# Kernel optimization log

Measured on AMD Instinct MI355X. Metric: run time of the kernel, lower is better.

The kernel has to match this reference:

```python
import jax, jax.numpy as jnp
import numpy as np

B, H, W, C, S, ITERS = 32, 80, 80, 32, 9, 3
HW = H * W
SCALE = C ** -0.5


def _grid(h, w):
    # matches SoftPositionEmbedding.build_grid: [1, h, w, 4] = [g, 1-g]
    r = jnp.stack(jnp.meshgrid(jnp.linspace(0., 1., h), jnp.linspace(0., 1., w), indexing='ij'), -1)
    return jnp.concatenate([r, 1. - r], -1)[None].astype(jnp.float32)


def _ln(x, g, b, ax):
    m = x.mean(ax, keepdims=True)
    v = x.var(ax, keepdims=True)
    return (x - m) / jnp.sqrt(v + 1e-5) * g + b


def _conv(x, w, b, p):
    y = jax.lax.conv_general_dilated(x, w, (1, 1), [(p, p), (p, p)],
                                     dimension_numbers=('NCHW', 'OIHW', 'NCHW'))
    return y + b[None, :, None, None]


def _convT(x, w, b, p):
    # stride-1 ConvTranspose2d == conv with spatially flipped kernel, pad k-1-p; w is [I,O,kh,kw]
    k = w.shape[-1]
    q = k - 1 - p
    y = jax.lax.conv_general_dilated(x, jnp.flip(w, (2, 3)), (1, 1), [(q, q), (q, q)],
                                     dimension_numbers=('NCHW', 'IOHW', 'NCHW'))
    return y + b[None, :, None, None]


def setup_inputs() -> dict:
    key = jax.random.key(0)
    ks = iter(jax.random.split(key, 64))

    def n(sh, s=0.05):
        return jax.random.normal(next(ks), sh, jnp.float32) * s

    return dict(
        x=jax.random.normal(next(ks), (B, 1, H, W), jnp.float32),
        slot_noise=jax.random.normal(next(ks), (B, S, C), jnp.float32),
        enc_w1=n((C, 1, 5, 5)), enc_b1=jnp.zeros((C,)),
        enc_w2=n((C, C, 5, 5)), enc_b2=jnp.zeros((C,)),
        enc_w3=n((C, C, 5, 5)), enc_b3=jnp.zeros((C,)),
        enc_w4=n((C, C, 5, 5)), enc_b4=jnp.zeros((C,)),
        pe_enc_w=n((C, 4)), pe_enc_b=jnp.zeros((C,)),
        ln_enc_g=jnp.ones((HW, C)), ln_enc_b=jnp.zeros((HW, C)),
        mlp_w1=n((C, C)), mlp_b1=jnp.zeros((C,)),
        mlp_w2=n((C, C)), mlp_b2=jnp.zeros((C,)),
        slots_mu=n((1, 1, C), 1.0), slots_sigma=jnp.abs(n((1, 1, C), 1.0)),
        ni_g=jnp.ones((C,)), ni_b=jnp.zeros((C,)),
        ns_g=jnp.ones((C,)), ns_b=jnp.zeros((C,)),
        q_w=n((C, C)), q_b=jnp.zeros((C,)),
        k_w=n((C, C)), k_b=jnp.zeros((C,)),
        v_w=n((C, C)), v_b=jnp.zeros((C,)),
        gru_wih=n((3 * C, C)), gru_whh=n((3 * C, C)),
        gru_bih=jnp.zeros((3 * C,)), gru_bhh=jnp.zeros((3 * C,)),
        res_ln_g=jnp.ones((C,)), res_ln_b=jnp.zeros((C,)),
        res_w1=n((C, C)), res_b1=jnp.zeros((C,)),
        res_w2=n((C, C)), res_b2=jnp.zeros((C,)),
        pe_dec_w=n((C, 4)), pe_dec_b=jnp.zeros((C,)),
        dec_w1=n((C, C, 5, 5)), dec_b1=jnp.zeros((C,)),
        dec_w2=n((C, C, 5, 5)), dec_b2=jnp.zeros((C,)),
        dec_w3=n((C, C, 5, 5)), dec_b3=jnp.zeros((C,)),
        dec_w4=n((C, 2, 3, 3)), dec_b4=jnp.zeros((2,)),
    )


def _forward(x, slot_noise, enc_w1, enc_b1, enc_w2, enc_b2, enc_w3, enc_b3, enc_w4, enc_b4,
             pe_enc_w, pe_enc_b, ln_enc_g, ln_enc_b, mlp_w1, mlp_b1, mlp_w2, mlp_b2,
             slots_mu, slots_sigma, ni_g, ni_b, ns_g, ns_b, q_w, q_b, k_w, k_b, v_w, v_b,
             gru_wih, gru_whh, gru_bih, gru_bhh, res_ln_g, res_ln_b, res_w1, res_b1,
             res_w2, res_b2, pe_dec_w, pe_dec_b, dec_w1, dec_b1, dec_w2, dec_b2,
             dec_w3, dec_b3, dec_w4, dec_b4):
    grid = _grid(H, W)  # [1,H,W,4]
    # --- conv encoder ---
    h = jax.nn.relu(_conv(x, enc_w1, enc_b1, 2))
    h = jax.nn.relu(_conv(h, enc_w2, enc_b2, 2))
    h = jax.nn.relu(_conv(h, enc_w3, enc_b3, 2))
    h = jax.nn.relu(_conv(h, enc_w4, enc_b4, 2))
    h = h.transpose(0, 2, 3, 1) + (grid @ pe_enc_w.T + pe_enc_b)  # soft pos emb
    h = h.reshape(B, HW, C)
    h = _ln(h, ln_enc_g, ln_enc_b, (-2, -1))  # LayerNorm([HW, C]): joint over last 2 dims
    h = jax.nn.relu(h @ mlp_w1.T + mlp_b1) @ mlp_w2.T + mlp_b2
    # --- slot attention ---
    slots = slots_mu + slots_sigma * slot_noise  # torch.normal(mu, sigma)
    xn = _ln(h, ni_g, ni_b, -1)
    keys = xn @ k_w.T + k_b
    values = xn @ v_w.T + v_b
    attn = None
    for _ in range(ITERS):
        prev = slots
        sn = _ln(slots, ns_g, ns_b, -1)
        q = sn @ q_w.T + q_b
        dots = jnp.einsum('bid,bjd->bij', q, keys) * SCALE  # [B,S,HW]
        attn = jax.nn.softmax(dots, axis=1) + 1e-8  # softmax over slots
        attn = attn / attn.sum(-1, keepdims=True)
        upd = jnp.einsum('bjd,bij->bid', values, attn)  # [B,S,C]
        # PyTorch GRUCell
        u2 = upd.reshape(-1, C)
        h2 = prev.reshape(-1, C)
        gx = u2 @ gru_wih.T + gru_bih
        gh = h2 @ gru_whh.T + gru_bhh
        xr, xz, xc = jnp.split(gx, 3, -1)
        hr, hz, hc = jnp.split(gh, 3, -1)
        r = jax.nn.sigmoid(xr + hr)
        z = jax.nn.sigmoid(xz + hz)
        cand = jnp.tanh(xc + r * hc)
        slots = ((1. - z) * cand + z * h2).reshape(B, S, C)
        res = _ln(slots, res_ln_g, res_ln_b, -1)
        res = jax.nn.relu(res @ res_w1.T + res_b1) @ res_w2.T + res_b2
        slots = slots + res
    # --- spatial-broadcast decoder ---
    d = jnp.broadcast_to(slots.reshape(B * S, 1, 1, C), (B * S, H, W, C))
    d = d + (grid @ pe_dec_w.T + pe_dec_b)
    d = d.transpose(0, 3, 1, 2)
    d = jax.nn.relu(_convT(d, dec_w1, dec_b1, 2))
    d = jax.nn.relu(_convT(d, dec_w2, dec_b2, 2))
    d = jax.nn.relu(_convT(d, dec_w3, dec_b3, 2))
    d = _convT(d, dec_w4, dec_b4, 1)
    d = d.transpose(0, 2, 3, 1).reshape(B, S, H, W, 2)
    recon, mlog = d[..., :1], d[..., 1:]
    mask = jax.nn.softmax(mlog, axis=1)  # over slots
    combined = (recon * mask).sum(1).transpose(0, 3, 1, 2)  # [B,1,H,W]
    return (combined, recon.transpose(0, 1, 4, 2, 3), mask.transpose(0, 1, 4, 2, 3),
            slots, attn.reshape(B, S, 1, H, W))


def reference(x, slot_noise, enc_w1, enc_b1, enc_w2, enc_b2, enc_w3, enc_b3, enc_w4, enc_b4,
              pe_enc_w, pe_enc_b, ln_enc_g, ln_enc_b, mlp_w1, mlp_b1, mlp_w2, mlp_b2,
              slots_mu, slots_sigma, ni_g, ni_b, ns_g, ns_b, q_w, q_b, k_w, k_b, v_w, v_b,
              gru_wih, gru_whh, gru_bih, gru_bhh, res_ln_g, res_ln_b, res_w1, res_b1,
              res_w2, res_b2, pe_dec_w, pe_dec_b, dec_w1, dec_b1, dec_w2, dec_b2,
              dec_w3, dec_b3, dec_w4, dec_b4):
    return _forward(x, slot_noise, enc_w1, enc_b1, enc_w2, enc_b2, enc_w3, enc_b3, enc_w4, enc_b4,
                    pe_enc_w, pe_enc_b, ln_enc_g, ln_enc_b, mlp_w1, mlp_b1, mlp_w2, mlp_b2,
                    slots_mu, slots_sigma, ni_g, ni_b, ns_g, ns_b, q_w, q_b, k_w, k_b, v_w, v_b,
                    gru_wih, gru_whh, gru_bih, gru_bhh, res_ln_g, res_ln_b, res_w1, res_b1,
                    res_w2, res_b2, pe_dec_w, pe_dec_b, dec_w1, dec_b1, dec_w2, dec_b2,
                    dec_w3, dec_b3, dec_w4, dec_b4)
```

## Files before the change

kernel.cpp:

```cpp
#include <hip/hip_runtime.h>
#include <cstddef>
#include <cstdint>


namespace {

constexpr int Bb  = 32;
constexpr int HWp = 6400;
constexpr float SCALEf = 0.17677669529663687f;

constexpr size_t O_COMB  = 0;
constexpr size_t O_RECON = 204800;
constexpr size_t O_MASK  = 2048000;
constexpr size_t O_SLOTS = 3891200;
constexpr size_t O_ATTN  = 3900416;

constexpr size_t W_PEENC = 0;
constexpr size_t W_PEDEC = 204800;
constexpr size_t W_BASE  = 409600;
constexpr size_t W_TC    = 512000;
constexpr size_t W_TS    = 537600;
constexpr size_t W_WP    = 768000;
constexpr size_t W_WPM   = 844800;
constexpr size_t W_LNPART= 846848;
constexpr size_t W_MEANR = 848448;
constexpr size_t W_Q     = 848512;
constexpr size_t W_SLOTS = 857728;
constexpr size_t W_APART = 866944;
constexpr size_t W_RSUM  = 874144;
constexpr size_t W_UP2   = 874432;
constexpr size_t W_KEYS  = 1104832;
constexpr size_t W_VALS  = 4381632;
constexpr size_t W_POOL  = 7658432;
constexpr size_t W_TOTAL = 29115328;

typedef __attribute__((ext_vector_type(8))) short short8;
typedef __attribute__((ext_vector_type(4))) float f32x4;

__device__ __forceinline__ ushort f2bf(float f) {
  uint u = __builtin_bit_cast(uint, f);
  uint r = (u + 0x7fffu + ((u >> 16) & 1u)) >> 16;
  return (ushort)r;
}
__device__ __forceinline__ float bf2f(ushort b) {
  uint u = ((uint)b) << 16;
  return __builtin_bit_cast(float, u);
}
__device__ __forceinline__ void unpk2(uint w, float& a, float& b) {
  a = __builtin_bit_cast(float, w << 16);
  b = __builtin_bit_cast(float, w & 0xffff0000u);
}

__device__ __forceinline__ void matvec32(const float* __restrict__ W,
                                         const float* __restrict__ bias,
                                         const float* x, float* y, bool relu) {
#pragma unroll
  for (int o = 0; o < 32; ++o) {
    float a = bias[o];
#pragma unroll
    for (int c = 0; c < 32; ++c) a = fmaf(x[c], W[o * 32 + c], a);
    y[o] = relu ? fmaxf(a, 0.f) : a;
  }
}

__device__ __forceinline__ float lane_ln(float v, int o, const float* __restrict__ g,
                                         const float* __restrict__ b) {
  float s = v;
#pragma unroll
  for (int m = 16; m >= 1; m >>= 1) s += __shfl_xor(s, m);
  float mean = s * (1.f / 32.f);
  float d = v - mean;
  float q = d * d;
#pragma unroll
  for (int m = 16; m >= 1; m >>= 1) q += __shfl_xor(q, m);
  float rstd = rsqrtf(q * (1.f / 32.f) + 1e-5f);
  return d * rstd * g[o] + b[o];
}


__global__ void k_pe_maps(const float* __restrict__ pew_e, const float* __restrict__ peb_e,
                          const float* __restrict__ pew_d, const float* __restrict__ peb_d,
                          float* __restrict__ pe_enc, float* __restrict__ pe_dec) {
  int hw = blockIdx.x * 256 + threadIdx.x;
  if (hw >= HWp) return;
  int y = hw / 80, x = hw % 80;
  float g0 = y * (1.f / 79.f), g1 = x * (1.f / 79.f);
  float g2 = 1.f - g0, g3 = 1.f - g1;
#pragma unroll
  for (int c = 0; c < 32; ++c) {
    pe_enc[(size_t)hw * 32 + c] = peb_e[c] + g0 * pew_e[c * 4] + g1 * pew_e[c * 4 + 1] +
                                  g2 * pew_e[c * 4 + 2] + g3 * pew_e[c * 4 + 3];
    pe_dec[(size_t)c * HWp + hw] = peb_d[c] + g0 * pew_d[c * 4] + g1 * pew_d[c * 4 + 1] +
                                   g2 * pew_d[c * 4 + 2] + g3 * pew_d[c * 4 + 3];
  }
}


__global__ void k_pack(const float* __restrict__ w, ushort* __restrict__ dst, int trans) {
  int tap = blockIdx.x;
  int grp = threadIdx.x >> 6, lane = threadIdx.x & 63;
  int ky = tap / 5, kx = tap % 5;
  int m = grp * 16 + (lane & 15);
  int kb = (lane >> 4) * 8;
  ushort* o = dst + ((size_t)(tap * 2 + grp) * 64 + lane) * 8;
#pragma unroll
  for (int j = 0; j < 8; ++j) {
    int k = kb + j;
    float v = trans ? w[(size_t)k * 800 + m * 25 + (4 - ky) * 5 + (4 - kx)]
                    : w[(size_t)m * 800 + k * 25 + ky * 5 + kx];
    o[j] = f2bf(v);
  }
}

__global__ void k_pack_mat(const float* __restrict__ w, ushort* __restrict__ dst) {
  int grp = threadIdx.x >> 6, lane = threadIdx.x & 63;
  int m = grp * 16 + (lane & 15), kb = (lane >> 4) * 8;
  ushort* o = dst + ((size_t)(grp * 64 + lane)) * 8;
#pragma unroll
  for (int j = 0; j < 8; ++j) o[j] = f2bf(w[m * 32 + kb + j]);
}


__global__ void k_prep_tc(const float* __restrict__ w, float* __restrict__ tc) {
  const int rep[5] = {0, 1, 40, 78, 79};
  int cls = blockIdx.x;
  int yc = cls / 5, xc = cls % 5;
  int ci = threadIdx.x >> 5, co = threadIdx.x & 31;
  int yr = rep[yc], xr = rep[xc];
  float s = 0.f;
#pragma unroll
  for (int ky = 0; ky < 5; ++ky) {
    if ((unsigned)(yr + ky - 2) >= 80u) continue;
#pragma unroll
    for (int kx = 0; kx < 5; ++kx) {
      if ((unsigned)(xr + kx - 2) >= 80u) continue;
      s += w[(size_t)ci * 800 + co * 25 + (4 - ky) * 5 + (4 - kx)];
    }
  }
  tc[(size_t)cls * 1024 + ci * 32 + co] = s;
}

__global__ void k_ts(const float* __restrict__ tc, const float* __restrict__ slots,
                     float* __restrict__ ts) {
  int idx = blockIdx.x * 256 + threadIdx.x;
  if (idx >= 288 * 800) return;
  int img = idx / 800, rem = idx % 800;
  int cls = rem >> 5, o = rem & 31;
  float s = 0.f;
#pragma unroll
  for (int ci = 0; ci < 32; ++ci)
    s += tc[(size_t)cls * 1024 + ci * 32 + o] * slots[(size_t)img * 32 + ci];
  ts[idx] = s;
}


template <int MODE, bool RELU>
__global__ __launch_bounds__(256, 2) void k_conv_mfma(
    const void* __restrict__ in_, const ushort* __restrict__ wp,
    const float* __restrict__ bias, ushort* __restrict__ out_,
    const float* __restrict__ ts, int n0) {
  __shared__ int4 sm[4032];
  const int n = blockIdx.y, rt = blockIdx.x;
  const int t = threadIdx.x;

  for (int i = t; i < 4032; i += 256) {
    int x = i % 84, ru = i / 84;
    int r = ru >> 2, u = ru & 3;
    int gy = rt * 8 + r - 2, gx = x - 2;
    int4 pk = {0, 0, 0, 0};
    if ((unsigned)gy < 80u && (unsigned)gx < 80u) {
      int hw = gy * 80 + gx;
      if constexpr (MODE == 0) {
        const float* fp = (const float*)in_;
        ushort bb[8];
#pragma unroll
        for (int j = 0; j < 8; ++j)
          bb[j] = f2bf(fp[(size_t)(u * 8 + j) * HWp + hw]);
        pk.x = (int)((uint)bb[0] | ((uint)bb[1] << 16));
        pk.y = (int)((uint)bb[2] | ((uint)bb[3] << 16));
        pk.z = (int)((uint)bb[4] | ((uint)bb[5] << 16));
        pk.w = (int)((uint)bb[6] | ((uint)bb[7] << 16));
      } else if constexpr (MODE == 1) {
        pk = *(const int4*)((const ushort*)in_ + ((size_t)n * HWp + hw) * 32 + u * 8);
      } else {
        int4 bp = *(const int4*)((const ushort*)in_ + (size_t)hw * 32 + u * 8);
        int yc = gy < 2 ? gy : (gy > 77 ? gy - 75 : 2);
        int xc = gx < 2 ? gx : (gx > 77 ? gx - 75 : 2);
        const float* tp = ts + ((size_t)(n0 + n) * 25 + (yc * 5 + xc)) * 32 + u * 8;
        float t0, t1;
        uint* pw = (uint*)&pk;
        const uint* bw = (const uint*)&bp;
#pragma unroll
        for (int h = 0; h < 4; ++h) {
          unpk2(bw[h], t0, t1);
          float f0 = fmaxf(t0 + tp[2 * h], 0.f);
          float f1 = fmaxf(t1 + tp[2 * h + 1], 0.f);
          pw[h] = (uint)f2bf(f0) | ((uint)f2bf(f1) << 16);
        }
      }
    }
    int up = u ^ ((x >> 1) & 3);
    sm[(r * 84 + x) * 4 + up] = pk;
  }
  __syncthreads();

  const int wv = t >> 6, lane = t & 63;
  const int l15 = lane & 15, lg = lane >> 4;
  const short8* smS = (const short8*)sm;

  f32x4 acc[2][5][2];
#pragma unroll
  for (int a = 0; a < 2; ++a)
#pragma unroll
    for (int b = 0; b < 5; ++b)
#pragma unroll
      for (int c = 0; c < 2; ++c) acc[a][b][c] = f32x4{0.f, 0.f, 0.f, 0.f};

  for (int dy = 0; dy < 5; ++dy) {
    for (int dx = 0; dx < 5; ++dx) {
      int tap = dy * 5 + dx;
      short8 A0 = *(const short8*)(wp + ((size_t)(tap * 2 + 0) * 64 + lane) * 8);
      short8 A1 = *(const short8*)(wp + ((size_t)(tap * 2 + 1) * 64 + lane) * 8);
#pragma unroll
      for (int ri = 0; ri < 2; ++ri) {
        int rbase = (wv * 2 + ri + dy) * 336;
#pragma unroll
        for (int xg = 0; xg < 5; ++xg) {
          int xs = xg * 16 + l15 + dx;
          short8 Bv = smS[rbase + xs * 4 + (lg ^ ((xs >> 1) & 3))];
          acc[ri][xg][0] = __builtin_amdgcn_mfma_f32_16x16x32_bf16(A0, Bv, acc[ri][xg][0], 0, 0, 0);
          acc[ri][xg][1] = __builtin_amdgcn_mfma_f32_16x16x32_bf16(A1, Bv, acc[ri][xg][1], 0, 0, 0);
        }
      }
    }
  }

  float bv[2][4];
#pragma unroll
  for (int cg = 0; cg < 2; ++cg)
#pragma unroll
    for (int q = 0; q < 4; ++q) bv[cg][q] = bias[cg * 16 + lg * 4 + q];
  int y0 = rt * 8 + wv * 2;
#pragma unroll
  for (int ri = 0; ri < 2; ++ri) {
#pragma unroll
    for (int xg = 0; xg < 5; ++xg) {
      size_t px = (size_t)n * HWp + (y0 + ri) * 80 + (xg * 16 + l15);
#pragma unroll
      for (int cg = 0; cg < 2; ++cg) {
        f32x4 v = acc[ri][xg][cg];
        float o0 = v[0] + bv[cg][0], o1 = v[1] + bv[cg][1];
        float o2 = v[2] + bv[cg][2], o3 = v[3] + bv[cg][3];
        if (RELU) {
          o0 = fmaxf(o0, 0.f); o1 = fmaxf(o1, 0.f);
          o2 = fmaxf(o2, 0.f); o3 = fmaxf(o3, 0.f);
        }
        uint2 pk;
        pk.x = (uint)f2bf(o0) | ((uint)f2bf(o1) << 16);
        pk.y = (uint)f2bf(o2) | ((uint)f2bf(o3) << 16);
        *(uint2*)(out_ + px * 32 + cg * 16 + lg * 4) = pk;
      }
    }
  }
}


__global__ __launch_bounds__(256) void k_conv1(const float* __restrict__ in,
                                               const float* __restrict__ w,
                                               const float* __restrict__ b,
                                               ushort* __restrict__ out) {
  int hw = blockIdx.x * 256 + threadIdx.x;
  int n = blockIdx.y;
  int y = hw / 80, x = hw % 80;
  float xv[25];
#pragma unroll
  for (int ky = 0; ky < 5; ++ky)
#pragma unroll
    for (int kx = 0; kx < 5; ++kx) {
      int iy = y + ky - 2, ix = x + kx - 2;
      xv[ky * 5 + kx] = ((unsigned)iy < 80u && (unsigned)ix < 80u)
                            ? in[(size_t)n * HWp + iy * 80 + ix] : 0.f;
    }
  float a[32];
#pragma unroll
  for (int co = 0; co < 32; ++co) {
    float s = b[co];
#pragma unroll
    for (int tp = 0; tp < 25; ++tp) s = fmaf(xv[tp], w[co * 25 + tp], s);
    a[co] = fmaxf(s, 0.f);
  }
  ushort* op = out + ((size_t)n * HWp + hw) * 32;
#pragma unroll
  for (int g = 0; g < 4; ++g) {
    uint4 pk;
    pk.x = (uint)f2bf(a[g * 8 + 0]) | ((uint)f2bf(a[g * 8 + 1]) << 16);
    pk.y = (uint)f2bf(a[g * 8 + 2]) | ((uint)f2bf(a[g * 8 + 3]) << 16);
    pk.z = (uint)f2bf(a[g * 8 + 4]) | ((uint)f2bf(a[g * 8 + 5]) << 16);
    pk.w = (uint)f2bf(a[g * 8 + 6]) | ((uint)f2bf(a[g * 8 + 7]) << 16);
    *(uint4*)(op + g * 8) = pk;
  }
}


__global__ __launch_bounds__(256) void k_conv4(const ushort* __restrict__ in,
                                               const float* __restrict__ w,
                                               const float* __restrict__ b,
                                               float* __restrict__ outR,
                                               float* __restrict__ outM, int n0) {
  __shared__ float sw[2 * 288];
  for (int e = threadIdx.x; e < 576; e += 256) {
    int co = e / 288, rem = e % 288;
    int tap = rem / 32, ci = rem % 32;
    sw[e] = w[(size_t)(ci * 2 + co) * 9 + 8 - tap];
  }
  __syncthreads();
  int hw = blockIdx.x * 256 + threadIdx.x;
  int nl = blockIdx.y;
  int y = hw / 80, x = hw % 80;
  float a0 = b[0], a1 = b[1];
  const ushort* ip = in + (size_t)nl * HWp * 32;
#pragma unroll
  for (int ky = 0; ky < 3; ++ky) {
#pragma unroll
    for (int kx = 0; kx < 3; ++kx) {
      int iy = y + ky - 1, ix = x + kx - 1;
      if ((unsigned)iy >= 80u || (unsigned)ix >= 80u) continue;
      int tap = ky * 3 + kx;
      const int4* p = (const int4*)(ip + (size_t)(iy * 80 + ix) * 32);
      const float* w0 = sw + tap * 32;
      const float* w1 = sw + 288 + tap * 32;
#pragma unroll
      for (int u = 0; u < 4; ++u) {
        int4 ch = p[u];
        const uint* cw = (const uint*)&ch;
#pragma unroll
        for (int h = 0; h < 4; ++h) {
          float v0, v1;
          unpk2(cw[h], v0, v1);
          int ci = u * 8 + h * 2;
          a0 = fmaf(v0, w0[ci], a0);     a1 = fmaf(v0, w1[ci], a1);
          a0 = fmaf(v1, w0[ci + 1], a0); a1 = fmaf(v1, w1[ci + 1], a1);
        }
      }
    }
  }
  outR[(size_t)(n0 + nl) * HWp + hw] = a0;
  outM[(size_t)(n0 + nl) * HWp + hw] = a1;
}


__global__ __launch_bounds__(256) void k_hstats(const ushort* __restrict__ enc,
                                                const float* __restrict__ pe_enc,
                                                float* __restrict__ lnpart) {
  int b = blockIdx.y;
  int hw = blockIdx.x * 256 + threadIdx.x;
  const int4* ep = (const int4*)(enc + ((size_t)b * HWp + hw) * 32);
  float v[32];
#pragma unroll
  for (int u = 0; u < 4; ++u) {
    int4 ch = ep[u];
    const uint* cw = (const uint*)&ch;
#pragma unroll
    for (int h = 0; h < 4; ++h) unpk2(cw[h], v[u * 8 + h * 2], v[u * 8 + h * 2 + 1]);
  }
  float s = 0.f, ss = 0.f;
#pragma unroll
  for (int c = 0; c < 32; ++c) {
    v[c] += pe_enc[(size_t)hw * 32 + c];
    s += v[c]; ss += v[c] * v[c];
  }
  __shared__ float r1[256], r2[256];
  r1[threadIdx.x] = s; r2[threadIdx.x] = ss;
  __syncthreads();
  for (int off = 128; off > 0; off >>= 1) {
    if (threadIdx.x < off) { r1[threadIdx.x] += r1[threadIdx.x + off]; r2[threadIdx.x] += r2[threadIdx.x + off]; }
    __syncthreads();
  }
  if (threadIdx.x == 0) {
    lnpart[(size_t)(b * 25 + blockIdx.x) * 2] = r1[0];
    lnpart[(size_t)(b * 25 + blockIdx.x) * 2 + 1] = r2[0];
  }
}

__global__ void k_statsfin(const float* __restrict__ lnpart, float* __restrict__ meanr) {
  int b = threadIdx.x;
  if (b >= 32) return;
  float s = 0.f, ss = 0.f;
  for (int k = 0; k < 25; ++k) {
    s += lnpart[(size_t)(b * 25 + k) * 2];
    ss += lnpart[(size_t)(b * 25 + k) * 2 + 1];
  }
  float m = s * (1.f / 204800.f);
  float var = ss * (1.f / 204800.f) - m * m;
  meanr[b * 2] = m;
  meanr[b * 2 + 1] = rsqrtf(var + 1e-5f);
}


__global__ __launch_bounds__(256) void k_lnmlpkv_mfma(
    const ushort* __restrict__ enc, const float* __restrict__ pe,
    const float* __restrict__ meanr,
    const float* __restrict__ g, const float* __restrict__ bb,
    const ushort* __restrict__ wm,
    const float* __restrict__ b1, const float* __restrict__ b2,
    const float* __restrict__ nig, const float* __restrict__ nib,
    const float* __restrict__ kb, const float* __restrict__ vb,
    ushort* __restrict__ keys, ushort* __restrict__ vals) {
  __shared__ ushort ls[256 * 32];
  const int b = blockIdx.y, jb = blockIdx.x;
  const int t = threadIdx.x, wv = t >> 6, lane = t & 63;
  const int l15 = lane & 15, lg = lane >> 4;
  const int skey = l15 & 3;

  short8 A[4][2];
#pragma unroll
  for (int mt = 0; mt < 4; ++mt)
#pragma unroll
    for (int gr = 0; gr < 2; ++gr)
      A[mt][gr] = *(const short8*)(wm + ((size_t)(mt * 2 + gr) * 64 + lane) * 8);

  float4 b1v0 = *(const float4*)(b1 + lg * 4),  b1v1 = *(const float4*)(b1 + 16 + lg * 4);
  float4 b2v0 = *(const float4*)(b2 + lg * 4),  b2v1 = *(const float4*)(b2 + 16 + lg * 4);
  float4 ng0  = *(const float4*)(nig + lg * 4), ng1  = *(const float4*)(nig + 16 + lg * 4);
  float4 nb0  = *(const float4*)(nib + lg * 4), nb1  = *(const float4*)(nib + 16 + lg * 4);
  float4 kbv0 = *(const float4*)(kb + lg * 4),  kbv1 = *(const float4*)(kb + 16 + lg * 4);
  float4 vbv0 = *(const float4*)(vb + lg * 4),  vbv1 = *(const float4*)(vb + 16 + lg * 4);

  const float m_ = meanr[b * 2], rs_ = meanr[b * 2 + 1];

  short8 bx[4];
#pragma unroll
  for (int g2 = 0; g2 < 4; ++g2) {
    int pos = jb * 256 + wv * 64 + g2 * 16 + l15;
    int4 e = *(const int4*)(enc + ((size_t)b * HWp + pos) * 32 + lg * 8);
    float xv[8];
    const uint* ew = (const uint*)&e;
#pragma unroll
    for (int h = 0; h < 4; ++h) unpk2(ew[h], xv[2 * h], xv[2 * h + 1]);
    float4 p0 = *(const float4*)(pe + (size_t)pos * 32 + lg * 8);
    float4 p1 = *(const float4*)(pe + (size_t)pos * 32 + lg * 8 + 4);
    float4 g0 = *(const float4*)(g + (size_t)pos * 32 + lg * 8);
    float4 g1 = *(const float4*)(g + (size_t)pos * 32 + lg * 8 + 4);
    float4 q0 = *(const float4*)(bb + (size_t)pos * 32 + lg * 8);
    float4 q1 = *(const float4*)(bb + (size_t)pos * 32 + lg * 8 + 4);
    float pv[8] = {p0.x, p0.y, p0.z, p0.w, p1.x, p1.y, p1.z, p1.w};
    float gv[8] = {g0.x, g0.y, g0.z, g0.w, g1.x, g1.y, g1.z, g1.w};
    float qv[8] = {q0.x, q0.y, q0.z, q0.w, q1.x, q1.y, q1.z, q1.w};
    uint pk[4];
#pragma unroll
    for (int h = 0; h < 4; ++h) {
      float f0 = (xv[2 * h] + pv[2 * h] - m_) * rs_ * gv[2 * h] + qv[2 * h];
      float f1 = (xv[2 * h + 1] + pv[2 * h + 1] - m_) * rs_ * gv[2 * h + 1] + qv[2 * h + 1];
      pk[h] = (uint)f2bf(f0) | ((uint)f2bf(f1) << 16);
    }
    bx[g2] = __builtin_bit_cast(short8, *(int4*)pk);
  }

  auto lds_write = [&](int posl, int cg, const f32x4& v) {
    int u = cg * 2 + (lg >> 1);
    int us = u ^ skey;
    uint2 pk;
    pk.x = (uint)f2bf(v[0]) | ((uint)f2bf(v[1]) << 16);
    pk.y = (uint)f2bf(v[2]) | ((uint)f2bf(v[3]) << 16);
    *(uint2*)(ls + (size_t)posl * 32 + us * 8 + (lg & 1) * 4) = pk;
  };

#pragma unroll
  for (int g2 = 0; g2 < 4; ++g2) {
    int posl = wv * 64 + g2 * 16 + l15;
    f32x4 a0 = __builtin_amdgcn_mfma_f32_16x16x32_bf16(A[0][0], bx[g2], f32x4{0, 0, 0, 0}, 0, 0, 0);
    f32x4 a1 = __builtin_amdgcn_mfma_f32_16x16x32_bf16(A[0][1], bx[g2], f32x4{0, 0, 0, 0}, 0, 0, 0);
    f32x4 r0, r1;
#pragma unroll
    for (int q = 0; q < 4; ++q) {
      r0[q] = fmaxf(a0[q] + (&b1v0.x)[q], 0.f);
      r1[q] = fmaxf(a1[q] + (&b1v1.x)[q], 0.f);
    }
    lds_write(posl, 0, r0);
    lds_write(posl, 1, r1);
  }
  __syncthreads();
  short8 t0f[4];
#pragma unroll
  for (int g2 = 0; g2 < 4; ++g2) {
    int posl = wv * 64 + g2 * 16 + l15;
    t0f[g2] = *(const short8*)(ls + (size_t)posl * 32 + (lg ^ skey) * 8);
  }
  __syncthreads();

#pragma unroll
  for (int g2 = 0; g2 < 4; ++g2) {
    int posl = wv * 64 + g2 * 16 + l15;
    f32x4 c0 = __builtin_amdgcn_mfma_f32_16x16x32_bf16(A[1][0], t0f[g2], f32x4{0, 0, 0, 0}, 0, 0, 0);
    f32x4 c1 = __builtin_amdgcn_mfma_f32_16x16x32_bf16(A[1][1], t0f[g2], f32x4{0, 0, 0, 0}, 0, 0, 0);
#pragma unroll
    for (int q = 0; q < 4; ++q) { c0[q] += (&b2v0.x)[q]; c1[q] += (&b2v1.x)[q]; }
    float s = 0.f;
#pragma unroll
    for (int q = 0; q < 4; ++q) s += c0[q] + c1[q];
    s += __shfl_xor(s, 16); s += __shfl_xor(s, 32);
    float mean = s * (1.f / 32.f);
    float var = 0.f;
#pragma unroll
    for (int q = 0; q < 4; ++q) {
      float d0 = c0[q] - mean, d1 = c1[q] - mean;
      var += d0 * d0 + d1 * d1;
    }
    var += __shfl_xor(var, 16); var += __shfl_xor(var, 32);
    float rstd = rsqrtf(var * (1.f / 32.f) + 1e-5f);
    f32x4 y0, y1;
#pragma unroll
    for (int q = 0; q < 4; ++q) {
      y0[q] = (c0[q] - mean) * rstd * (&ng0.x)[q] + (&nb0.x)[q];
      y1[q] = (c1[q] - mean) * rstd * (&ng1.x)[q] + (&nb1.x)[q];
    }
    lds_write(posl, 0, y0);
    lds_write(posl, 1, y1);
  }
  __syncthreads();
  short8 xnf[4];
#pragma unroll
  for (int g2 = 0; g2 < 4; ++g2) {
    int posl = wv * 64 + g2 * 16 + l15;
    xnf[g2] = *(const short8*)(ls + (size_t)posl * 32 + (lg ^ skey) * 8);
  }

#pragma unroll
  for (int g2 = 0; g2 < 4; ++g2) {
    int pos = jb * 256 + wv * 64 + g2 * 16 + l15;
    size_t px = ((size_t)b * HWp + pos) * 32;
    f32x4 k0 = __builtin_amdgcn_mfma_f32_16x16x32_bf16(A[2][0], xnf[g2], f32x4{0, 0, 0, 0}, 0, 0, 0);
    f32x4 k1 = __builtin_amdgcn_mfma_f32_16x16x32_bf16(A[2][1], xnf[g2], f32x4{0, 0, 0, 0}, 0, 0, 0);
    f32x4 v0 = __builtin_amdgcn_mfma_f32_16x16x32_bf16(A[3][0], xnf[g2], f32x4{0, 0, 0, 0}, 0, 0, 0);
    f32x4 v1 = __builtin_amdgcn_mfma_f32_16x16x32_bf16(A[3][1], xnf[g2], f32x4{0, 0, 0, 0}, 0, 0, 0);
    uint2 pk;
    pk.x = (uint)f2bf(k0[0] + kbv0.x) | ((uint)f2bf(k0[1] + kbv0.y) << 16);
    pk.y = (uint)f2bf(k0[2] + kbv0.z) | ((uint)f2bf(k0[3] + kbv0.w) << 16);
    *(uint2*)(keys + px + lg * 4) = pk;
    pk.x = (uint)f2bf(k1[0] + kbv1.x) | ((uint)f2bf(k1[1] + kbv1.y) << 16);
    pk.y = (uint)f2bf(k1[2] + kbv1.z) | ((uint)f2bf(k1[3] + kbv1.w) << 16);
    *(uint2*)(keys + px + 16 + lg * 4) = pk;
    pk.x = (uint)f2bf(v0[0] + vbv0.x) | ((uint)f2bf(v0[1] + vbv0.y) << 16);
    pk.y = (uint)f2bf(v0[2] + vbv0.z) | ((uint)f2bf(v0[3] + vbv0.w) << 16);
    *(uint2*)(vals + px + lg * 4) = pk;
    pk.x = (uint)f2bf(v1[0] + vbv1.x) | ((uint)f2bf(v1[1] + vbv1.y) << 16);
    pk.y = (uint)f2bf(v1[2] + vbv1.z) | ((uint)f2bf(v1[3] + vbv1.w) << 16);
    *(uint2*)(vals + px + 16 + lg * 4) = pk;
  }
}


__global__ __launch_bounds__(256) void k_init_q(
    const float* __restrict__ mu, const float* __restrict__ sig,
    const float* __restrict__ noise,
    const float* __restrict__ nsg, const float* __restrict__ nsb,
    const float* __restrict__ qw, const float* __restrict__ qb,
    float* __restrict__ slots, float* __restrict__ qbuf) {
  int rl = threadIdx.x >> 5, o = threadIdx.x & 31;
  int r = blockIdx.x * 8 + rl;
  float s = mu[o] + sig[o] * noise[(size_t)r * 32 + o];
  slots[(size_t)r * 32 + o] = s;
  float y = lane_ln(s, o, nsg, nsb);
  __shared__ float S[8][32];
  S[rl][o] = y;
  __syncthreads();
  float qv = qb[o];
#pragma unroll
  for (int c = 0; c < 32; ++c) qv = fmaf(S[rl][c], qw[o * 32 + c], qv);
  qbuf[(size_t)r * 32 + o] = qv;
}

template <bool LAST>
__global__ __launch_bounds__(256) void k_dots_upd(
    const float* __restrict__ qbuf, const ushort* __restrict__ keys,
    const ushort* __restrict__ vals, float* __restrict__ attnt,
    float* __restrict__ apart, float* __restrict__ up2) {
  int b = blockIdx.y, jb = blockIdx.x;
  int t = threadIdx.x;
  int j = jb * 256 + t;
  __shared__ float qs[288];
  __shared__ float aL[2304];
  __shared__ float wr[36];
  for (int e = t; e < 288; e += 256) qs[e] = qbuf[(size_t)b * 288 + e];
  __syncthreads();
  float k[32];
  const int4* kp = (const int4*)(keys + ((size_t)b * HWp + j) * 32);
#pragma unroll
  for (int u = 0; u < 4; ++u) {
    int4 ch = kp[u];
    const uint* cw = (const uint*)&ch;
#pragma unroll
    for (int h = 0; h < 4; ++h) unpk2(cw[h], k[u * 8 + h * 2], k[u * 8 + h * 2 + 1]);
  }
  float d[9];
#pragma unroll
  for (int i = 0; i < 9; ++i) {
    float a = 0.f;
#pragma unroll
    for (int c = 0; c < 32; ++c) a = fmaf(qs[i * 32 + c], k[c], a);
    d[i] = a * SCALEf;
  }
  float mx = d[0];
#pragma unroll
  for (int i = 1; i < 9; ++i) mx = fmaxf(mx, d[i]);
  float sum = 0.f;
#pragma unroll
  for (int i = 0; i < 9; ++i) { d[i] = __expf(d[i] - mx); sum += d[i]; }
  float inv = 1.f / sum;
  float a9[9];
#pragma unroll
  for (int i = 0; i < 9; ++i) {
    a9[i] = d[i] * inv + 1e-8f;
    if (LAST) attnt[((size_t)b * 9 + i) * HWp + j] = a9[i];
    aL[t * 9 + i] = a9[i];
  }
  int lane = t & 63, wid = t >> 6;
#pragma unroll
  for (int i = 0; i < 9; ++i) {
    float v = a9[i];
    for (int off = 32; off > 0; off >>= 1) v += __shfl_down(v, off);
    if (lane == 0) wr[wid * 9 + i] = v;
  }
  __syncthreads();
  if (t < 9)
    apart[(size_t)(b * 9 + t) * 25 + jb] = wr[t] + wr[9 + t] + wr[18 + t] + wr[27 + t];
  int c = t & 31, g = t >> 5;
  float acc[9];
#pragma unroll
  for (int i = 0; i < 9; ++i) acc[i] = 0.f;
  const ushort* vp = vals + ((size_t)b * HWp + jb * 256) * 32 + c;
  for (int jj = g; jj < 256; jj += 8) {
    float v = bf2f(vp[(size_t)jj * 32]);
#pragma unroll
    for (int i = 0; i < 9; ++i) acc[i] = fmaf(v, aL[jj * 9 + i], acc[i]);
  }
  __syncthreads();
#pragma unroll
  for (int i = 0; i < 9; ++i) aL[(i * 8 + g) * 32 + c] = acc[i];
  __syncthreads();
  for (int i = g; i < 9; i += 8) {
    float s = 0.f;
#pragma unroll
    for (int g2 = 0; g2 < 8; ++g2) s += aL[(i * 8 + g2) * 32 + c];
    up2[(((size_t)b * 25 + jb) * 9 + i) * 32 + c] = s;
  }
}

__global__ __launch_bounds__(256) void k_gru_fused(
    const float* __restrict__ up2, const float* __restrict__ apart,
    float* __restrict__ slots, float* __restrict__ rowsum, float* __restrict__ qbuf,
    const float* __restrict__ wih, const float* __restrict__ whh,
    const float* __restrict__ bih, const float* __restrict__ bhh,
    const float* __restrict__ rlg, const float* __restrict__ rlb,
    const float* __restrict__ rw1, const float* __restrict__ rb1,
    const float* __restrict__ rw2, const float* __restrict__ rb2,
    const float* __restrict__ nsg, const float* __restrict__ nsb,
    const float* __restrict__ qw, const float* __restrict__ qb) {
  int rl = threadIdx.x >> 5, o = threadIdx.x & 31;
  int r = blockIdx.x * 8 + rl;
  int b = r / 9, i = r - b * 9;

  float rs = 0.f;
#pragma unroll
  for (int k = 0; k < 25; ++k) rs += apart[(size_t)(b * 9 + i) * 25 + k];
  if (o == 0) rowsum[r] = rs;

  float uo = 0.f;
#pragma unroll
  for (int jc = 0; jc < 25; ++jc) uo += up2[(((size_t)b * 25 + jc) * 9 + i) * 32 + o];
  uo /= rs;
  float ho = slots[(size_t)r * 32 + o];

  __shared__ float Us[8][32], Hs[8][32];
  Us[rl][o] = uo; Hs[rl][o] = ho;
  __syncthreads();

  float xr = bih[o], xz = bih[32 + o], xc = bih[64 + o];
  float hr = bhh[o], hz = bhh[32 + o], hc = bhh[64 + o];
#pragma unroll
  for (int c = 0; c < 32; ++c) {
    float u = Us[rl][c], h = Hs[rl][c];
    xr = fmaf(u, wih[o * 32 + c], xr);          hr = fmaf(h, whh[o * 32 + c], hr);
    xz = fmaf(u, wih[(32 + o) * 32 + c], xz);   hz = fmaf(h, whh[(32 + o) * 32 + c], hz);
    xc = fmaf(u, wih[(64 + o) * 32 + c], xc);   hc = fmaf(h, whh[(64 + o) * 32 + c], hc);
  }
  float rr = 1.f / (1.f + __expf(-(xr + hr)));
  float zz = 1.f / (1.f + __expf(-(xz + hz)));
  float cand = tanhf(xc + rr * hc);
  float sm = (1.f - zz) * cand + zz * ho;

  float y = lane_ln(sm, o, rlg, rlb);
  __syncthreads();
  Us[rl][o] = y;
  __syncthreads();
  float t1 = rb1[o];
#pragma unroll
  for (int c = 0; c < 32; ++c) t1 = fmaf(Us[rl][c], rw1[o * 32 + c], t1);
  t1 = fmaxf(t1, 0.f);
  Hs[rl][o] = t1;
  __syncthreads();
  float res = rb2[o];
#pragma unroll
  for (int c = 0; c < 32; ++c) res = fmaf(Hs[rl][c], rw2[o * 32 + c], res);
  float ns = sm + res;
  slots[(size_t)r * 32 + o] = ns;

  float y2 = lane_ln(ns, o, nsg, nsb);
  __syncthreads();
  Us[rl][o] = y2;
  __syncthreads();
  float qv = qb[o];
#pragma unroll
  for (int c = 0; c < 32; ++c) qv = fmaf(Us[rl][c], qw[o * 32 + c], qv);
  qbuf[(size_t)r * 32 + o] = qv;
}


__global__ void k_attn_out(const float* __restrict__ attnt, const float* __restrict__ rsum,
                           float* __restrict__ out) {
  size_t idx = (size_t)blockIdx.x * 256 + threadIdx.x;
  out[O_ATTN + idx] = attnt[idx] / rsum[idx / HWp];
}

__global__ void k_slots_out(const float* __restrict__ slots, float* __restrict__ out) {
  int idx = blockIdx.x * 256 + threadIdx.x;
  if (idx < 9216) out[O_SLOTS + idx] = slots[idx];
}

__global__ __launch_bounds__(256) void k_final(float* __restrict__ out) {
  int b = blockIdx.y;
  int j = blockIdx.x * 256 + threadIdx.x;
  float r[9], ml[9];
#pragma unroll
  for (int s = 0; s < 9; ++s) {
    r[s]  = out[O_RECON + (size_t)(b * 9 + s) * HWp + j];
    ml[s] = out[O_MASK  + (size_t)(b * 9 + s) * HWp + j];
  }
  float mx = ml[0];
#pragma unroll
  for (int s = 1; s < 9; ++s) mx = fmaxf(mx, ml[s]);
  float sum = 0.f;
#pragma unroll
  for (int s = 0; s < 9; ++s) { ml[s] = __expf(ml[s] - mx); sum += ml[s]; }
  float inv = 1.f / sum;
  float comb = 0.f;
#pragma unroll
  for (int s = 0; s < 9; ++s) {
    float mk = ml[s] * inv;
    comb = fmaf(r[s], mk, comb);
    out[O_MASK + (size_t)(b * 9 + s) * HWp + j] = mk;
  }
  out[O_COMB + (size_t)b * HWp + j] = comb;
}

}


extern "C" void kernel_launch(void* const* d_in, const int* in_sizes, int n_in,
                              void* d_out, int out_size, void* d_ws, size_t ws_size,
                              hipStream_t stream) {
  if (ws_size < W_TOTAL * sizeof(float)) return;

  const float* in_x       = (const float*)d_in[0];
  const float* slot_noise = (const float*)d_in[1];
  const float* enc_w1 = (const float*)d_in[2];   const float* enc_b1 = (const float*)d_in[3];
  const float* enc_w2 = (const float*)d_in[4];   const float* enc_b2 = (const float*)d_in[5];
  const float* enc_w3 = (const float*)d_in[6];   const float* enc_b3 = (const float*)d_in[7];
  const float* enc_w4 = (const float*)d_in[8];   const float* enc_b4 = (const float*)d_in[9];
  const float* pe_enc_w = (const float*)d_in[10]; const float* pe_enc_b = (const float*)d_in[11];
  const float* ln_enc_g = (const float*)d_in[12]; const float* ln_enc_b = (const float*)d_in[13];
  const float* mlp_w1 = (const float*)d_in[14];  const float* mlp_b1 = (const float*)d_in[15];
  const float* mlp_w2 = (const float*)d_in[16];  const float* mlp_b2 = (const float*)d_in[17];
  const float* slots_mu = (const float*)d_in[18]; const float* slots_sigma = (const float*)d_in[19];
  const float* ni_g = (const float*)d_in[20];    const float* ni_b = (const float*)d_in[21];
  const float* ns_g = (const float*)d_in[22];    const float* ns_b = (const float*)d_in[23];
  const float* q_w = (const float*)d_in[24];     const float* q_b = (const float*)d_in[25];
  const float* k_w = (const float*)d_in[26];     const float* k_b = (const float*)d_in[27];
  const float* v_w = (const float*)d_in[28];     const float* v_b = (const float*)d_in[29];
  const float* gru_wih = (const float*)d_in[30]; const float* gru_whh = (const float*)d_in[31];
  const float* gru_bih = (const float*)d_in[32]; const float* gru_bhh = (const float*)d_in[33];
  const float* res_ln_g = (const float*)d_in[34]; const float* res_ln_b = (const float*)d_in[35];
  const float* res_w1 = (const float*)d_in[36];  const float* res_b1 = (const float*)d_in[37];
  const float* res_w2 = (const float*)d_in[38];  const float* res_b2 = (const float*)d_in[39];
  const float* pe_dec_w = (const float*)d_in[40]; const float* pe_dec_b = (const float*)d_in[41];
  const float* dec_w1 = (const float*)d_in[42];  const float* dec_b1 = (const float*)d_in[43];
  const float* dec_w2 = (const float*)d_in[44];  const float* dec_b2 = (const float*)d_in[45];
  const float* dec_w3 = (const float*)d_in[46];  const float* dec_b3 = (const float*)d_in[47];
  const float* dec_w4 = (const float*)d_in[48];  const float* dec_b4 = (const float*)d_in[49];

  float* ws  = (float*)d_ws;
  float* out = (float*)d_out;
  ushort* wp  = (ushort*)(ws + W_WP);
  ushort* wpm = (ushort*)(ws + W_WPM);

  k_pe_maps<<<dim3(25), 256, 0, stream>>>(pe_enc_w, pe_enc_b, pe_dec_w, pe_dec_b,
                                          ws + W_PEENC, ws + W_PEDEC);

  const size_t WPSTR = 25 * 2 * 64 * 8;
  k_pack<<<dim3(25), 128, 0, stream>>>(enc_w2, wp + 0 * WPSTR, 0);
  k_pack<<<dim3(25), 128, 0, stream>>>(enc_w3, wp + 1 * WPSTR, 0);
  k_pack<<<dim3(25), 128, 0, stream>>>(enc_w4, wp + 2 * WPSTR, 0);
  k_pack<<<dim3(25), 128, 0, stream>>>(dec_w1, wp + 3 * WPSTR, 1);
  k_pack<<<dim3(25), 128, 0, stream>>>(dec_w2, wp + 4 * WPSTR, 1);
  k_pack<<<dim3(25), 128, 0, stream>>>(dec_w3, wp + 5 * WPSTR, 1);
  k_pack_mat<<<dim3(1), 128, 0, stream>>>(mlp_w1, wpm + 0 * 1024);
  k_pack_mat<<<dim3(1), 128, 0, stream>>>(mlp_w2, wpm + 1 * 1024);
  k_pack_mat<<<dim3(1), 128, 0, stream>>>(k_w,   wpm + 2 * 1024);
  k_pack_mat<<<dim3(1), 128, 0, stream>>>(v_w,   wpm + 3 * 1024);
  k_prep_tc<<<dim3(25), 1024, 0, stream>>>(dec_w1, ws + W_TC);

  ushort* base  = (ushort*)(ws + W_BASE);
  ushort* keys  = (ushort*)(ws + W_KEYS);
  ushort* vals  = (ushort*)(ws + W_VALS);
  float*  attnt = ws + W_POOL;
  ushort* E1    = (ushort*)(ws + W_POOL);
  ushort* E2    = (ushort*)(ws + W_POOL + 3276800);

  k_conv_mfma<0, false><<<dim3(10, 1), 256, 0, stream>>>(
      ws + W_PEDEC, wp + 3 * WPSTR, dec_b1, base, nullptr, 0);

  k_conv1<<<dim3(25, Bb), 256, 0, stream>>>(in_x, enc_w1, enc_b1, E1);
  k_conv_mfma<1, true><<<dim3(10, Bb), 256, 0, stream>>>(E1, wp + 0 * WPSTR, enc_b2, E2, nullptr, 0);
  k_conv_mfma<1, true><<<dim3(10, Bb), 256, 0, stream>>>(E2, wp + 1 * WPSTR, enc_b3, E1, nullptr, 0);
  k_conv_mfma<1, true><<<dim3(10, Bb), 256, 0, stream>>>(E1, wp + 2 * WPSTR, enc_b4, E2, nullptr, 0);

  k_hstats<<<dim3(25, Bb), 256, 0, stream>>>(E2, ws + W_PEENC, ws + W_LNPART);
  k_statsfin<<<dim3(1), 64, 0, stream>>>(ws + W_LNPART, ws + W_MEANR);
  k_lnmlpkv_mfma<<<dim3(25, Bb), 256, 0, stream>>>(E2, ws + W_PEENC, ws + W_MEANR,
                                                   ln_enc_g, ln_enc_b, wpm,
                                                   mlp_b1, mlp_b2, ni_g, ni_b,
                                                   k_b, v_b, keys, vals);

  k_init_q<<<dim3(36), 256, 0, stream>>>(slots_mu, slots_sigma, slot_noise,
                                         ns_g, ns_b, q_w, q_b, ws + W_SLOTS, ws + W_Q);
  for (int it = 0; it < 3; ++it) {
    if (it == 2)
      k_dots_upd<true><<<dim3(25, Bb), 256, 0, stream>>>(ws + W_Q, keys, vals, attnt,
                                                         ws + W_APART, ws + W_UP2);
    else
      k_dots_upd<false><<<dim3(25, Bb), 256, 0, stream>>>(ws + W_Q, keys, vals, attnt,
                                                          ws + W_APART, ws + W_UP2);
    k_gru_fused<<<dim3(36), 256, 0, stream>>>(ws + W_UP2, ws + W_APART,
                                              ws + W_SLOTS, ws + W_RSUM, ws + W_Q,
                                              gru_wih, gru_whh, gru_bih, gru_bhh,
                                              res_ln_g, res_ln_b, res_w1, res_b1,
                                              res_w2, res_b2, ns_g, ns_b, q_w, q_b);
  }
  k_attn_out<<<dim3(7200), 256, 0, stream>>>(attnt, ws + W_RSUM, out);
  k_slots_out<<<dim3(36), 256, 0, stream>>>(ws + W_SLOTS, out);

  k_ts<<<dim3(900), 256, 0, stream>>>(ws + W_TC, ws + W_SLOTS, ws + W_TS);

  ushort* XA = (ushort*)(ws + W_POOL);
  ushort* XB = XA + (size_t)96 * 32 * HWp;
  for (int ch = 0; ch < 3; ++ch) {
    int n0 = ch * 96;
    k_conv_mfma<2, true><<<dim3(10, 96), 256, 0, stream>>>(base, wp + 4 * WPSTR, dec_b2, XA,
                                                           ws + W_TS, n0);
    k_conv_mfma<1, true><<<dim3(10, 96), 256, 0, stream>>>(XA, wp + 5 * WPSTR, dec_b3, XB,
                                                           nullptr, 0);
    k_conv4<<<dim3(25, 96), 256, 0, stream>>>(XB, dec_w4, dec_b4,
                                              out + O_RECON, out + O_MASK, n0);
  }

  k_final<<<dim3(25, Bb), 256, 0, stream>>>(out);
}
```

Measured before the change: 637.0 us.

## Retile MFMA conv into 16x16 spatial tiles with smaller LDS footprint

Changes the 5x5 MFMA convolution from 8-row full-width strips (84-wide halo, 64KB LDS) to 16x16 output tiles with a 20x20 halo (25KB LDS), giving each wave 4 rows of 16 pixels. This shrinks per-block LDS and accumulators so launch bounds can request 4 blocks per CU, and it raises the grid from 10 to 25 blocks per image. The trade-off is a larger halo overhead (400 vs 336 staged pixels per 256 outputs) and less weight reuse per loaded tap. An unused matvec helper is also removed.

```diff
diff --git a/kernel.cpp b/kernel.cpp
--- a/kernel.cpp
+++ b/kernel.cpp
@@ -51,18 +51,6 @@
   b = __builtin_bit_cast(float, w & 0xffff0000u);
 }
 
-__device__ __forceinline__ void matvec32(const float* __restrict__ W,
-                                         const float* __restrict__ bias,
-                                         const float* x, float* y, bool relu) {
-#pragma unroll
-  for (int o = 0; o < 32; ++o) {
-    float a = bias[o];
-#pragma unroll
-    for (int c = 0; c < 32; ++c) a = fmaf(x[c], W[o * 32 + c], a);
-    y[o] = relu ? fmaxf(a, 0.f) : a;
-  }
-}
-
 __device__ __forceinline__ float lane_ln(float v, int o, const float* __restrict__ g,
                                          const float* __restrict__ b) {
   float s = v;
@@ -155,18 +143,19 @@
 
 
 template <int MODE, bool RELU>
-__global__ __launch_bounds__(256, 2) void k_conv_mfma(
+__global__ __launch_bounds__(256, 4) void k_conv_mfma(
     const void* __restrict__ in_, const ushort* __restrict__ wp,
     const float* __restrict__ bias, ushort* __restrict__ out_,
     const float* __restrict__ ts, int n0) {
-  __shared__ int4 sm[4032];
-  const int n = blockIdx.y, rt = blockIdx.x;
+  __shared__ int4 sm[1600];
+  const int n = blockIdx.y;
+  const int ty = blockIdx.x / 5, tx = blockIdx.x % 5;
   const int t = threadIdx.x;
 
-  for (int i = t; i < 4032; i += 256) {
-    int x = i % 84, ru = i / 84;
-    int r = ru >> 2, u = ru & 3;
-    int gy = rt * 8 + r - 2, gx = x - 2;
+  for (int i = t; i < 1600; i += 256) {
+    int u = i & 3, px = i >> 2;
+    int x = px % 20, r = px / 20;
+    int gy = ty * 16 + r - 2, gx = tx * 16 + x - 2;
     int4 pk = {0, 0, 0, 0};
     if ((unsigned)gy < 80u && (unsigned)gx < 80u) {
       int hw = gy * 80 + gx;
@@ -200,7 +189,7 @@
       }
     }
     int up = u ^ ((x >> 1) & 3);
-    sm[(r * 84 + x) * 4 + up] = pk;
+    sm[(r * 20 + x) * 4 + up] = pk;
   }
   __syncthreads();
 
@@ -208,29 +197,28 @@
   const int l15 = lane & 15, lg = lane >> 4;
   const short8* smS = (const short8*)sm;
 
-  f32x4 acc[2][5][2];
-#pragma unroll
-  for (int a = 0; a < 2; ++a)
-#pragma unroll
-    for (int b = 0; b < 5; ++b)
-#pragma unroll
-      for (int c = 0; c < 2; ++c) acc[a][b][c] = f32x4{0.f, 0.f, 0.f, 0.f};
-
+  f32x4 acc[4][2];
+#pragma unroll
+  for (int o = 0; o < 4; ++o)
+#pragma unroll
+    for (int c = 0; c < 2; ++c) acc[o][c] = f32x4{0.f, 0.f, 0.f, 0.f};
+
+  const int xs = l15;
+#pragma unroll
   for (int dy = 0; dy < 5; ++dy) {
+#pragma unroll
     for (int dx = 0; dx < 5; ++dx) {
       int tap = dy * 5 + dx;
       short8 A0 = *(const short8*)(wp + ((size_t)(tap * 2 + 0) * 64 + lane) * 8);
       short8 A1 = *(const short8*)(wp + ((size_t)(tap * 2 + 1) * 64 + lane) * 8);
-#pragma unroll
-      for (int ri = 0; ri < 2; ++ri) {
-        int rbase = (wv * 2 + ri + dy) * 336;
-#pragma unroll
-        for (int xg = 0; xg < 5; ++xg) {
-          int xs = xg * 16 + l15 + dx;
-          short8 Bv = smS[rbase + xs * 4 + (lg ^ ((xs >> 1) & 3))];
-          acc[ri][xg][0] = __builtin_amdgcn_mfma_f32_16x16x32_bf16(A0, Bv, acc[ri][xg][0], 0, 0, 0);
-          acc[ri][xg][1] = __builtin_amdgcn_mfma_f32_16x16x32_bf16(A1, Bv, acc[ri][xg][1], 0, 0, 0);
-        }
+      int xx = xs + dx;
+      int us = lg ^ ((xx >> 1) & 3);
+#pragma unroll
+      for (int o = 0; o < 4; ++o) {
+        int srow = wv * 4 + o + dy;
+        short8 Bv = smS[(srow * 20 + xx) * 4 + us];
+        acc[o][0] = __builtin_amdgcn_mfma_f32_16x16x32_bf16(A0, Bv, acc[o][0], 0, 0, 0);
+        acc[o][1] = __builtin_amdgcn_mfma_f32_16x16x32_bf16(A1, Bv, acc[o][1], 0, 0, 0);
       }
     }
   }
@@ -240,26 +228,23 @@
   for (int cg = 0; cg < 2; ++cg)
 #pragma unroll
     for (int q = 0; q < 4; ++q) bv[cg][q] = bias[cg * 16 + lg * 4 + q];
-  int y0 = rt * 8 + wv * 2;
-#pragma unroll
-  for (int ri = 0; ri < 2; ++ri) {
-#pragma unroll
-    for (int xg = 0; xg < 5; ++xg) {
-      size_t px = (size_t)n * HWp + (y0 + ri) * 80 + (xg * 16 + l15);
-#pragma unroll
-      for (int cg = 0; cg < 2; ++cg) {
-        f32x4 v = acc[ri][xg][cg];
-        float o0 = v[0] + bv[cg][0], o1 = v[1] + bv[cg][1];
-        float o2 = v[2] + bv[cg][2], o3 = v[3] + bv[cg][3];
-        if (RELU) {
-          o0 = fmaxf(o0, 0.f); o1 = fmaxf(o1, 0.f);
-          o2 = fmaxf(o2, 0.f); o3 = fmaxf(o3, 0.f);
-        }
-        uint2 pk;
-        pk.x = (uint)f2bf(o0) | ((uint)f2bf(o1) << 16);
-        pk.y = (uint)f2bf(o2) | ((uint)f2bf(o3) << 16);
-        *(uint2*)(out_ + px * 32 + cg * 16 + lg * 4) = pk;
+  const int ybase = ty * 16 + wv * 4, xbase = tx * 16 + l15;
+#pragma unroll
+  for (int o = 0; o < 4; ++o) {
+    size_t px = (size_t)n * HWp + (ybase + o) * 80 + xbase;
+#pragma unroll
+    for (int cg = 0; cg < 2; ++cg) {
+      f32x4 v = acc[o][cg];
+      float o0 = v[0] + bv[cg][0], o1 = v[1] + bv[cg][1];
+      float o2 = v[2] + bv[cg][2], o3 = v[3] + bv[cg][3];
+      if (RELU) {
+        o0 = fmaxf(o0, 0.f); o1 = fmaxf(o1, 0.f);
+        o2 = fmaxf(o2, 0.f); o3 = fmaxf(o3, 0.f);
       }
+      uint2 pk;
+      pk.x = (uint)f2bf(o0) | ((uint)f2bf(o1) << 16);
+      pk.y = (uint)f2bf(o2) | ((uint)f2bf(o3) << 16);
+      *(uint2*)(out_ + px * 32 + cg * 16 + lg * 4) = pk;
     }
   }
 }
@@ -816,13 +801,13 @@
   ushort* E1    = (ushort*)(ws + W_POOL);
   ushort* E2    = (ushort*)(ws + W_POOL + 3276800);
 
-  k_conv_mfma<0, false><<<dim3(10, 1), 256, 0, stream>>>(
+  k_conv_mfma<0, false><<<dim3(25, 1), 256, 0, stream>>>(
       ws + W_PEDEC, wp + 3 * WPSTR, dec_b1, base, nullptr, 0);
 
   k_conv1<<<dim3(25, Bb), 256, 0, stream>>>(in_x, enc_w1, enc_b1, E1);
-  k_conv_mfma<1, true><<<dim3(10, Bb), 256, 0, stream>>>(E1, wp + 0 * WPSTR, enc_b2, E2, nullptr, 0);
-  k_conv_mfma<1, true><<<dim3(10, Bb), 256, 0, stream>>>(E2, wp + 1 * WPSTR, enc_b3, E1, nullptr, 0);
-  k_conv_mfma<1, true><<<dim3(10, Bb), 256, 0, stream>>>(E1, wp + 2 * WPSTR, enc_b4, E2, nullptr, 0);
+  k_conv_mfma<1, true><<<dim3(25, Bb), 256, 0, stream>>>(E1, wp + 0 * WPSTR, enc_b2, E2, nullptr, 0);
+  k_conv_mfma<1, true><<<dim3(25, Bb), 256, 0, stream>>>(E2, wp + 1 * WPSTR, enc_b3, E1, nullptr, 0);
+  k_conv_mfma<1, true><<<dim3(25, Bb), 256, 0, stream>>>(E1, wp + 2 * WPSTR, enc_b4, E2, nullptr, 0);
 
   k_hstats<<<dim3(25, Bb), 256, 0, stream>>>(E2, ws + W_PEENC, ws + W_LNPART);
   k_statsfin<<<dim3(1), 64, 0, stream>>>(ws + W_LNPART, ws + W_MEANR);
@@ -855,9 +840,9 @@
   ushort* XB = XA + (size_t)96 * 32 * HWp;
   for (int ch = 0; ch < 3; ++ch) {
     int n0 = ch * 96;
-    k_conv_mfma<2, true><<<dim3(10, 96), 256, 0, stream>>>(base, wp + 4 * WPSTR, dec_b2, XA,
+    k_conv_mfma<2, true><<<dim3(25, 96), 256, 0, stream>>>(base, wp + 4 * WPSTR, dec_b2, XA,
                                                            ws + W_TS, n0);
-    k_conv_mfma<1, true><<<dim3(10, 96), 256, 0, stream>>>(XA, wp + 5 * WPSTR, dec_b3, XB,
+    k_conv_mfma<1, true><<<dim3(25, 96), 256, 0, stream>>>(XA, wp + 5 * WPSTR, dec_b3, XB,
                                                            nullptr, 0);
     k_conv4<<<dim3(25, 96), 256, 0, stream>>>(XB, dec_w4, dec_b4,
                                               out + O_RECON, out + O_MASK, n0);
```

Result: faster. 582.2 us (-8.6%).
